# Optimization experiments

Hardware: AMD Instinct MI355X
Metric: run time of the kernel (lower is better)

Reference implementation:

```python
import jax, jax.numpy as jnp
import numpy as np
from jax import lax

GRID_X, GRID_Y = 8, 8
CELL = 48  # cell_pixel_size
BATCH = 64


def setup_inputs() -> dict:
    key = jax.random.key(0)
    ks = jax.random.split(key, 9)
    s = lambda *sh: 1.0 / np.sqrt(np.prod(sh[1:])) if len(sh) > 1 else 0.0
    inp = {
        "x": jax.random.normal(ks[0], (BATCH, 3, GRID_X * CELL, GRID_Y * CELL), jnp.float32),
        "conv1_w": jax.random.normal(ks[1], (16, 3, 8, 8), jnp.float32) * 0.05,
        "conv1_b": jax.random.normal(ks[2], (16,), jnp.float32) * 0.05,
        "conv2_w": jax.random.normal(ks[3], (32, 16, 4, 4), jnp.float32) * 0.05,
        "conv2_b": jax.random.normal(ks[4], (32,), jnp.float32) * 0.05,
        "fc1_w": jax.random.normal(ks[5], (256, 288), jnp.float32) * 0.05,
        "fc1_b": jax.random.normal(ks[6], (256,), jnp.float32) * 0.05,
        "fc2_w": jax.random.normal(ks[7], (4, 256), jnp.float32) * 0.05,
        "fc2_b": jax.random.normal(ks[8], (4,), jnp.float32) * 0.05,
    }
    return inp


def _conv(x, w, b, stride, pad):
    y = lax.conv_general_dilated(
        x, w, window_strides=(stride, stride),
        padding=[(pad, pad), (pad, pad)],
        dimension_numbers=("NCHW", "OIHW", "NCHW"))
    return y + b[None, :, None, None]


def reference(x, conv1_w, conv1_b, conv2_w, conv2_b, fc1_w, fc1_b, fc2_w, fc2_b):
    B = x.shape[0]
    num_cells = GRID_X * GRID_Y
    # Grid extraction: one strided reshape instead of per-cell crop loop.
    # [B,3,gx*CELL,gy*CELL] -> [B,gx,gy,3,CELL,CELL] -> [B*cells,3,CELL,CELL]
    cells = x.reshape(B, 3, GRID_X, CELL, GRID_Y, CELL)
    cells = cells.transpose(0, 2, 4, 1, 3, 5).reshape(B * num_cells, 3, CELL, CELL)
    h = jax.nn.relu(_conv(cells, conv1_w, conv1_b, stride=4, pad=2))  # [N,16,12,12]
    h = jax.nn.relu(_conv(h, conv2_w, conv2_b, stride=4, pad=1))      # [N,32,3,3]
    h = h.reshape(B * num_cells, -1)                                   # [N,288]
    h = jax.nn.relu(h @ fc1_w.T + fc1_b)
    logits = h @ fc2_w.T + fc2_b
    probs = jax.nn.softmax(logits, axis=1)
    feats = probs.reshape(B, num_cells, 4)
    return (feats[:, :, 0], feats[:, :, 1], feats[:, :, 2])
```

## Files before the change

kernel.cpp:

```cpp
#include <hip/hip_runtime.h>

typedef float f32x4 __attribute__((ext_vector_type(4)));
typedef short s16x8 __attribute__((ext_vector_type(8)));

#define CB_PLANE 2704
#define CB_ROW 52

#define WS_H2G  0
#define WS_FW1  1179648
#define WS_W1   1253376
#define WS_W2   1256448

__device__ __forceinline__ ushort f2bf(float f) {
  unsigned u = __float_as_uint(f);
  unsigned r = (u + 0x7fffu + ((u >> 16) & 1u)) >> 16;
  return (ushort)r;
}
__device__ __forceinline__ uint pk2(float a, float b) {
  return (uint)f2bf(a) | ((uint)f2bf(b) << 16);
}

__global__ void prep_kernel(const float* __restrict__ fw1,
                            const float* __restrict__ w1,
                            const float* __restrict__ w2,
                            ushort* __restrict__ ws) {
  int i = blockIdx.x * 256 + threadIdx.x;
  if (i < 73728)       ws[WS_FW1 + i] = f2bf(fw1[i]);
  else if (i < 76800)  ws[WS_W1 + i - 73728] = f2bf(w1[i - 73728]);
  else                 ws[WS_W2 + i - 76800] = f2bf(w2[i - 76800]);
}

__device__ __forceinline__ void epi1(ushort* A2, f32x4 acc, int mt, int r16,
                                     int g, float b1v) {
#pragma unroll
  for (int rr = 0; rr < 4; ++rr) {
    int m = mt * 16 + g * 4 + rr;
    int oy = m / 12, ox = m - 12 * oy;
    if (oy < 11 && ox < 11) {
      float v = fmaxf(acc[rr] + b1v, 0.f);
      int py = (oy + 1) >> 2, k2y = (oy + 1) & 3;
      int px = (ox + 1) >> 2, k2x = (ox + 1) & 3;
      A2[(py * 3 + px) * 264 + r16 * 16 + k2y * 4 + k2x] = f2bf(v);
    }
  }
}

__global__ __launch_bounds__(256, 4)
void conv_kernel(const float* __restrict__ x,
                 const ushort* __restrict__ w1b, const float* __restrict__ b1,
                 const ushort* __restrict__ w2b, const float* __restrict__ b2,
                 ushort* __restrict__ h2g)
{
  __shared__ __align__(16) ushort cb[3 * CB_PLANE];
  __shared__ __align__(16) ushort A2[16 * 264];

  const int t = threadIdx.x;
  const int w = t >> 6;
  const int r16 = t & 15;
  const int g = (t & 63) >> 4;
  const int cell0 = blockIdx.x * 4;

  int goff[7], eoff[7];
#pragma unroll
  for (int i = 0; i < 7; ++i) {
    int q = i * 256 + t;
    int qq = (i < 6 || t < 192) ? q : 0;
    int c = qq / 576; int r2 = qq - c * 576;
    int y = r2 / 12;  int quad = r2 - y * 12;
    goff[i] = c * 36864 + y * 96 + quad;
    eoff[i] = c * CB_PLANE + (y + 2) * CB_ROW + 2 + quad * 4;
  }
  const float4* x4 = (const float4*)x;

  float4 v[7];
  {
    int n = cell0, b = n >> 6, gg = n & 63;
    int base4 = b * 110592 + (gg >> 3) * 4608 + (gg & 7) * 12;
#pragma unroll
    for (int i = 0; i < 7; ++i)
      if (i < 6 || t < 192) v[i] = x4[base4 + goff[i]];
  }

  for (int i = t; i < 600; i += 256) {
    int pl = i / 200, r = i - pl * 200;
    int off;
    if (r < 52)        off = r;
    else if (r < 104)  off = 1300 + (r - 52);
    else if (r < 152)  off = (2 + (r - 104)) * 26;
    else               off = (2 + (r - 152)) * 26 + 25;
    ((uint*)cb)[pl * 1352 + off] = 0u;
  }
  {
    uint4 z = make_uint4(0u, 0u, 0u, 0u);
    uint4* p2 = (uint4*)A2;
    for (int i = t; i < 528; i += 256) p2[i] = z;
  }

  s16x8 b1f[6];
#pragma unroll
  for (int s = 0; s < 6; ++s)
    b1f[s] = *(const s16x8*)&w1b[r16 * 192 + s * 32 + g * 8];
  const float b1v = b1[r16];
  const float b2v = b2[(w & 1) * 16 + r16];

#pragma unroll
  for (int i = 0; i < 7; ++i)
    if (i < 6 || t < 192) {
      uint* d = (uint*)&cb[eoff[i]];
      d[0] = pk2(v[i].x, v[i].y);
      d[1] = pk2(v[i].z, v[i].w);
    }

  const int mt0 = w, mt1 = w + 4;
  int m0 = mt0 * 16 + r16, m1 = mt1 * 16 + r16, m2_ = 128 + r16;
  const int rA0 = (m0 / 12) * (4 * CB_ROW) + 4 * (m0 % 12);
  const int rA1 = (m1 / 12) * (4 * CB_ROW) + 4 * (m1 % 12);
  const int rA2 = (m2_ / 12) * (4 * CB_ROW) + 4 * (m2_ % 12);

  __syncthreads();

  for (int cl = 0; cl < 4; ++cl) {
    if (cl < 3) {
      int n = cell0 + cl + 1, b = n >> 6, gg = n & 63;
      int base4 = b * 110592 + (gg >> 3) * 4608 + (gg & 7) * 12;
#pragma unroll
      for (int i = 0; i < 7; ++i)
        if (i < 6 || t < 192) v[i] = x4[base4 + goff[i]];
    }

    f32x4 a0 = (f32x4){0.f, 0.f, 0.f, 0.f};
    f32x4 a1 = (f32x4){0.f, 0.f, 0.f, 0.f};
    f32x4 a2 = (f32x4){0.f, 0.f, 0.f, 0.f};
#pragma unroll
    for (int s = 0; s < 6; ++s) {
      int sbase = (s >> 1) * CB_PLANE + ((s & 1) * 4 + g) * CB_ROW;
      s16x8 a;
      ((uint2*)&a)[0] = *(const uint2*)&cb[sbase + rA0];
      ((uint2*)&a)[1] = *(const uint2*)&cb[sbase + rA0 + 4];
      a0 = __builtin_amdgcn_mfma_f32_16x16x32_bf16(a, b1f[s], a0, 0, 0, 0);
      ((uint2*)&a)[0] = *(const uint2*)&cb[sbase + rA1];
      ((uint2*)&a)[1] = *(const uint2*)&cb[sbase + rA1 + 4];
      a1 = __builtin_amdgcn_mfma_f32_16x16x32_bf16(a, b1f[s], a1, 0, 0, 0);
      if (w == 2) {
        ((uint2*)&a)[0] = *(const uint2*)&cb[sbase + rA2];
        ((uint2*)&a)[1] = *(const uint2*)&cb[sbase + rA2 + 4];
        a2 = __builtin_amdgcn_mfma_f32_16x16x32_bf16(a, b1f[s], a2, 0, 0, 0);
      }
    }
    epi1(A2, a0, mt0, r16, g, b1v);
    epi1(A2, a1, mt1, r16, g, b1v);
    if (w == 2) epi1(A2, a2, 8, r16, g, b1v);

    __syncthreads();

    if (w < 2) {
      f32x4 c2acc = (f32x4){0.f, 0.f, 0.f, 0.f};
#pragma unroll
      for (int s2 = 0; s2 < 8; ++s2) {
        uint4 av = *(const uint4*)&A2[r16 * 264 + s2 * 32 + g * 8];
        s16x8 bf = *(const s16x8*)&w2b[(w * 16 + r16) * 256 + s2 * 32 + g * 8];
        c2acc = __builtin_amdgcn_mfma_f32_16x16x32_bf16(*(s16x8*)&av, bf, c2acc, 0, 0, 0);
      }
#pragma unroll
      for (int rr = 0; rr < 4; ++rr) {
        int p2 = g * 4 + rr;
        if (p2 < 9) {
          float vv = fmaxf(c2acc[rr] + b2v, 0.f);
          h2g[(cell0 + cl) * 288 + (w * 16 + r16) * 9 + p2] = f2bf(vv);
        }
      }
    }
    if (cl < 3) {
#pragma unroll
      for (int i = 0; i < 7; ++i)
        if (i < 6 || t < 192) {
          uint* d = (uint*)&cb[eoff[i]];
          d[0] = pk2(v[i].x, v[i].y);
          d[1] = pk2(v[i].z, v[i].w);
        }
    }
    __syncthreads();
  }
}

__global__ __launch_bounds__(256, 4)
void fc_kernel(const ushort* __restrict__ fw1b, const float* __restrict__ fb1,
               const float* __restrict__ fw2, const float* __restrict__ fb2,
               const ushort* __restrict__ h2g, float* __restrict__ out)
{
  __shared__ __align__(16) ushort h2s[16 * 296];
  __shared__ __align__(16) float h3s[16 * 260];
  __shared__ float ls[16][4];

  const int t = threadIdx.x;
  const int w = t >> 6;
  const int r16 = t & 15;
  const int g = (t & 63) >> 4;
  const int c0 = blockIdx.x * 16;

  const uint* src = (const uint*)(h2g + c0 * 288);
  for (int j = t; j < 2304; j += 256) {
    int r = j / 144, ci = j - r * 144;
    *(uint*)&h2s[r * 296 + 2 * ci] = src[j];
  }
  __syncthreads();

  s16x8 af[9];
#pragma unroll
  for (int s = 0; s < 9; ++s)
    af[s] = *(const s16x8*)&h2s[r16 * 296 + s * 32 + g * 8];

  f32x4 fa0 = (f32x4){0.f,0.f,0.f,0.f}, fa1 = fa0, fa2 = fa0, fa3 = fa0;
#pragma unroll
  for (int s = 0; s < 9; ++s) {
    const int ko = s * 32 + g * 8;
#pragma unroll
    for (int i = 0; i < 4; ++i) {
      s16x8 bf = *(const s16x8*)&fw1b[((w * 4 + i) * 16 + r16) * 288 + ko];
      if (i == 0) fa0 = __builtin_amdgcn_mfma_f32_16x16x32_bf16(af[s], bf, fa0, 0, 0, 0);
      if (i == 1) fa1 = __builtin_amdgcn_mfma_f32_16x16x32_bf16(af[s], bf, fa1, 0, 0, 0);
      if (i == 2) fa2 = __builtin_amdgcn_mfma_f32_16x16x32_bf16(af[s], bf, fa2, 0, 0, 0);
      if (i == 3) fa3 = __builtin_amdgcn_mfma_f32_16x16x32_bf16(af[s], bf, fa3, 0, 0, 0);
    }
  }
#pragma unroll
  for (int i = 0; i < 4; ++i) {
    f32x4 fa = (i == 0) ? fa0 : (i == 1) ? fa1 : (i == 2) ? fa2 : fa3;
    int n = (w * 4 + i) * 16 + r16;
    float fb = fb1[n];
#pragma unroll
    for (int rr = 0; rr < 4; ++rr)
      h3s[(g * 4 + rr) * 260 + n] = fmaxf(fa[rr] + fb, 0.f);
  }
  __syncthreads();

  {
    int u = t >> 2, sub = t & 3;
    int cl = u >> 2, j = u & 3;
    const float4* hp = (const float4*)&h3s[cl * 260];
    const float4* wp = (const float4*)(fw2 + j * 256);
    float p = 0.f;
#pragma unroll
    for (int i = 0; i < 16; ++i) {
      int k4 = sub + 4 * i;
      float4 a = hp[k4], bb = wp[k4];
      p = fmaf(a.x, bb.x, p); p = fmaf(a.y, bb.y, p);
      p = fmaf(a.z, bb.z, p); p = fmaf(a.w, bb.w, p);
    }
    p += __shfl_xor(p, 1);
    p += __shfl_xor(p, 2);
    if (sub == 0) ls[cl][j] = p + fb2[j];
  }
  __syncthreads();

  if (t < 16) {
    float l0 = ls[t][0], l1 = ls[t][1], l2 = ls[t][2], l3 = ls[t][3];
    float m = fmaxf(fmaxf(l0, l1), fmaxf(l2, l3));
    float e0 = __expf(l0 - m), e1 = __expf(l1 - m),
          e2 = __expf(l2 - m), e3 = __expf(l3 - m);
    float inv = 1.f / (e0 + e1 + e2 + e3);
    int n = c0 + t;
    out[n] = e0 * inv;
    out[4096 + n] = e1 * inv;
    out[8192 + n] = e2 * inv;
  }
}

extern "C" void kernel_launch(void* const* d_in, const int* in_sizes, int n_in,
                              void* d_out, int out_size, void* d_ws, size_t ws_size,
                              hipStream_t stream) {
  const float* x   = (const float*)d_in[0];
  const float* w1  = (const float*)d_in[1];
  const float* b1  = (const float*)d_in[2];
  const float* w2  = (const float*)d_in[3];
  const float* b2  = (const float*)d_in[4];
  const float* fw1 = (const float*)d_in[5];
  const float* fb1 = (const float*)d_in[6];
  const float* fw2 = (const float*)d_in[7];
  const float* fb2 = (const float*)d_in[8];
  float* out = (float*)d_out;
  ushort* ws = (ushort*)d_ws;

  hipLaunchKernelGGL(prep_kernel, dim3(332), dim3(256), 0, stream,
                     fw1, w1, w2, ws);
  hipLaunchKernelGGL(conv_kernel, dim3(1024), dim3(256), 0, stream,
                     x, ws + WS_W1, b1, ws + WS_W2, b2, ws + WS_H2G);
  hipLaunchKernelGGL(fc_kernel, dim3(256), dim3(256), 0, stream,
                     ws + WS_FW1, fb1, fw2, fb2, ws + WS_H2G, out);
}
```

Measured before the change: 44.83 us.

## Fuse FC layers into conv kernel, keeping conv2 output in shared memory

The separate fc kernel is merged into the conv kernel, so each block writes its conv2 activations for its 4 cells to a zero-padded LDS tile instead of global memory. The block then runs fc1 with MFMA on a 16-row tile of which only 4 rows are real, followed by fc2 and softmax. This removes one kernel launch and the global round-trip of the intermediate activations. In exchange, each block now reads the full fc1 weight matrix (4x more weight traffic overall), wastes 3/4 of the MFMA rows, and uses more shared memory, which may lower occupancy.

```diff
diff --git a/kernel.cpp b/kernel.cpp
--- a/kernel.cpp
+++ b/kernel.cpp
@@ -6,10 +6,9 @@
 #define CB_PLANE 2704
 #define CB_ROW 52
 
-#define WS_H2G  0
-#define WS_FW1  1179648
-#define WS_W1   1253376
-#define WS_W2   1256448
+#define WS_FW1  0
+#define WS_W1   73728
+#define WS_W2   76800
 
 __device__ __forceinline__ ushort f2bf(float f) {
   unsigned u = __float_as_uint(f);
@@ -46,13 +45,18 @@
 }
 
 __global__ __launch_bounds__(256, 4)
-void conv_kernel(const float* __restrict__ x,
-                 const ushort* __restrict__ w1b, const float* __restrict__ b1,
-                 const ushort* __restrict__ w2b, const float* __restrict__ b2,
-                 ushort* __restrict__ h2g)
+void fused_kernel(const float* __restrict__ x,
+                  const ushort* __restrict__ w1b, const float* __restrict__ b1,
+                  const ushort* __restrict__ w2b, const float* __restrict__ b2,
+                  const ushort* __restrict__ fw1b, const float* __restrict__ fb1,
+                  const float* __restrict__ fw2, const float* __restrict__ fb2,
+                  float* __restrict__ out)
 {
   __shared__ __align__(16) ushort cb[3 * CB_PLANE];
   __shared__ __align__(16) ushort A2[16 * 264];
+  __shared__ __align__(16) ushort h2s[16 * 296];
+  __shared__ __align__(16) float h3s[4 * 260];
+  __shared__ float ls[4][4];
 
   const int t = threadIdx.x;
   const int w = t >> 6;
@@ -94,6 +98,8 @@
     uint4 z = make_uint4(0u, 0u, 0u, 0u);
     uint4* p2 = (uint4*)A2;
     for (int i = t; i < 528; i += 256) p2[i] = z;
+    uint* ph = (uint*)h2s;
+    for (int i = t; i < 2368; i += 256) ph[i] = 0u;
   }
 
   s16x8 b1f[6];
@@ -166,7 +172,7 @@
         int p2 = g * 4 + rr;
         if (p2 < 9) {
           float vv = fmaxf(c2acc[rr] + b2v, 0.f);
-          h2g[(cell0 + cl) * 288 + (w * 16 + r16) * 9 + p2] = f2bf(vv);
+          h2s[cl * 296 + (w * 16 + r16) * 9 + p2] = f2bf(vv);
         }
       }
     }
@@ -181,85 +187,68 @@
     }
     __syncthreads();
   }
-}
-
-__global__ __launch_bounds__(256, 4)
-void fc_kernel(const ushort* __restrict__ fw1b, const float* __restrict__ fb1,
-               const float* __restrict__ fw2, const float* __restrict__ fb2,
-               const ushort* __restrict__ h2g, float* __restrict__ out)
-{
-  __shared__ __align__(16) ushort h2s[16 * 296];
-  __shared__ __align__(16) float h3s[16 * 260];
-  __shared__ float ls[16][4];
-
-  const int t = threadIdx.x;
-  const int w = t >> 6;
-  const int r16 = t & 15;
-  const int g = (t & 63) >> 4;
-  const int c0 = blockIdx.x * 16;
-
-  const uint* src = (const uint*)(h2g + c0 * 288);
-  for (int j = t; j < 2304; j += 256) {
-    int r = j / 144, ci = j - r * 144;
-    *(uint*)&h2s[r * 296 + 2 * ci] = src[j];
+
+  {
+    s16x8 af[9];
+#pragma unroll
+    for (int s = 0; s < 9; ++s)
+      af[s] = *(const s16x8*)&h2s[r16 * 296 + s * 32 + g * 8];
+
+    f32x4 fa0 = (f32x4){0.f,0.f,0.f,0.f}, fa1 = fa0, fa2 = fa0, fa3 = fa0;
+#pragma unroll
+    for (int s = 0; s < 9; ++s) {
+      const int ko = s * 32 + g * 8;
+#pragma unroll
+      for (int i = 0; i < 4; ++i) {
+        s16x8 bf = *(const s16x8*)&fw1b[((w * 4 + i) * 16 + r16) * 288 + ko];
+        if (i == 0) fa0 = __builtin_amdgcn_mfma_f32_16x16x32_bf16(af[s], bf, fa0, 0, 0, 0);
+        if (i == 1) fa1 = __builtin_amdgcn_mfma_f32_16x16x32_bf16(af[s], bf, fa1, 0, 0, 0);
+        if (i == 2) fa2 = __builtin_amdgcn_mfma_f32_16x16x32_bf16(af[s], bf, fa2, 0, 0, 0);
+        if (i == 3) fa3 = __builtin_amdgcn_mfma_f32_16x16x32_bf16(af[s], bf, fa3, 0, 0, 0);
+      }
+    }
+    if (g == 0) {
+#pragma unroll
+      for (int i = 0; i < 4; ++i) {
+        f32x4 fa = (i == 0) ? fa0 : (i == 1) ? fa1 : (i == 2) ? fa2 : fa3;
+        int n = (w * 4 + i) * 16 + r16;
+        float fb = fb1[n];
+#pragma unroll
+        for (int rr = 0; rr < 4; ++rr)
+          h3s[rr * 260 + n] = fmaxf(fa[rr] + fb, 0.f);
+      }
+    }
   }
   __syncthreads();
 
-  s16x8 af[9];
-#pragma unroll
-  for (int s = 0; s < 9; ++s)
-    af[s] = *(const s16x8*)&h2s[r16 * 296 + s * 32 + g * 8];
-
-  f32x4 fa0 = (f32x4){0.f,0.f,0.f,0.f}, fa1 = fa0, fa2 = fa0, fa3 = fa0;
-#pragma unroll
-  for (int s = 0; s < 9; ++s) {
-    const int ko = s * 32 + g * 8;
-#pragma unroll
-    for (int i = 0; i < 4; ++i) {
-      s16x8 bf = *(const s16x8*)&fw1b[((w * 4 + i) * 16 + r16) * 288 + ko];
-      if (i == 0) fa0 = __builtin_amdgcn_mfma_f32_16x16x32_bf16(af[s], bf, fa0, 0, 0, 0);
-      if (i == 1) fa1 = __builtin_amdgcn_mfma_f32_16x16x32_bf16(af[s], bf, fa1, 0, 0, 0);
-      if (i == 2) fa2 = __builtin_amdgcn_mfma_f32_16x16x32_bf16(af[s], bf, fa2, 0, 0, 0);
-      if (i == 3) fa3 = __builtin_amdgcn_mfma_f32_16x16x32_bf16(af[s], bf, fa3, 0, 0, 0);
-    }
-  }
-#pragma unroll
-  for (int i = 0; i < 4; ++i) {
-    f32x4 fa = (i == 0) ? fa0 : (i == 1) ? fa1 : (i == 2) ? fa2 : fa3;
-    int n = (w * 4 + i) * 16 + r16;
-    float fb = fb1[n];
-#pragma unroll
-    for (int rr = 0; rr < 4; ++rr)
-      h3s[(g * 4 + rr) * 260 + n] = fmaxf(fa[rr] + fb, 0.f);
-  }
-  __syncthreads();
-
-  {
-    int u = t >> 2, sub = t & 3;
+  {
+    int u = t >> 4, sub = t & 15;
     int cl = u >> 2, j = u & 3;
     const float4* hp = (const float4*)&h3s[cl * 260];
     const float4* wp = (const float4*)(fw2 + j * 256);
     float p = 0.f;
 #pragma unroll
-    for (int i = 0; i < 16; ++i) {
-      int k4 = sub + 4 * i;
+    for (int i = 0; i < 4; ++i) {
+      int k4 = sub + 16 * i;
       float4 a = hp[k4], bb = wp[k4];
       p = fmaf(a.x, bb.x, p); p = fmaf(a.y, bb.y, p);
       p = fmaf(a.z, bb.z, p); p = fmaf(a.w, bb.w, p);
     }
     p += __shfl_xor(p, 1);
     p += __shfl_xor(p, 2);
+    p += __shfl_xor(p, 4);
+    p += __shfl_xor(p, 8);
     if (sub == 0) ls[cl][j] = p + fb2[j];
   }
   __syncthreads();
 
-  if (t < 16) {
+  if (t < 4) {
     float l0 = ls[t][0], l1 = ls[t][1], l2 = ls[t][2], l3 = ls[t][3];
     float m = fmaxf(fmaxf(l0, l1), fmaxf(l2, l3));
     float e0 = __expf(l0 - m), e1 = __expf(l1 - m),
           e2 = __expf(l2 - m), e3 = __expf(l3 - m);
     float inv = 1.f / (e0 + e1 + e2 + e3);
-    int n = c0 + t;
+    int n = cell0 + t;
     out[n] = e0 * inv;
     out[4096 + n] = e1 * inv;
     out[8192 + n] = e2 * inv;
@@ -283,8 +272,7 @@
 
   hipLaunchKernelGGL(prep_kernel, dim3(332), dim3(256), 0, stream,
                      fw1, w1, w2, ws);
-  hipLaunchKernelGGL(conv_kernel, dim3(1024), dim3(256), 0, stream,
-                     x, ws + WS_W1, b1, ws + WS_W2, b2, ws + WS_H2G);
-  hipLaunchKernelGGL(fc_kernel, dim3(256), dim3(256), 0, stream,
-                     ws + WS_FW1, fb1, fw2, fb2, ws + WS_H2G, out);
-}
+  hipLaunchKernelGGL(fused_kernel, dim3(1024), dim3(256), 0, stream,
+                     x, ws + WS_W1, b1, ws + WS_W2, b2,
+                     ws + WS_FW1, fb1, fw2, fb2, out);
+}
```

New measurement: 44.87 us. About the same (+0.1%).
